# Performance work log

Hardware: AMD Instinct MI355X
Metric: run time of the kernel (lower is better)

The kernel has to match this reference:

```python
import jax, jax.numpy as jnp
import numpy as np

N_NODES = 100000
N_EDGES = 1600000
D_IN = 64
HID = 64


def setup_inputs() -> dict:
    key = jax.random.key(0)
    ks = jax.random.split(key, 8)
    s = 0.1  # modest weight scale
    return {
        "x": jax.random.normal(ks[0], (N_NODES, D_IN), jnp.float32),
        "edge_index": jax.random.randint(ks[1], (2, N_EDGES), 0, N_NODES),
        "W1": jax.random.normal(ks[2], (D_IN, HID), jnp.float32) * s,
        "b1": jnp.zeros((HID,), jnp.float32),
        "W2": jax.random.normal(ks[3], (HID, HID), jnp.float32) * s,
        "b2": jnp.zeros((HID,), jnp.float32),
        "fc1_w": jax.random.normal(ks[4], (HID, 256), jnp.float32) * s,
        "fc1_b": jnp.zeros((256,), jnp.float32),
        "fc2_w": jax.random.normal(ks[5], (256, 1), jnp.float32) * s,
        "fc2_b": jnp.zeros((1,), jnp.float32),
    }


def reference(x, edge_index, W1, b1, W2, b2, fc1_w, fc1_b, fc2_w, fc2_b):
    N = x.shape[0]
    loop = jnp.arange(N, dtype=edge_index.dtype)
    # GCNConv default: add self-loops + symmetric D^{-1/2}(A+I)D^{-1/2} normalization
    row = jnp.concatenate([edge_index[0], loop])  # source nodes
    col = jnp.concatenate([edge_index[1], loop])  # target nodes
    deg = jax.ops.segment_sum(jnp.ones(row.shape[0], x.dtype), col, num_segments=N)
    dinv = jnp.where(deg > 0, jax.lax.rsqrt(deg), 0.0)
    norm = dinv[row] * dinv[col]  # [E+N]

    def gcn_conv(h, W, b):
        h = h @ W                                   # [N, H] transform first
        msg = h[row] * norm[:, None]                # gather + scale, [E+N, H]
        return jax.ops.segment_sum(msg, col, num_segments=N) + b

    # dropout is inactive in eval mode (training=False)
    h = jax.nn.relu(gcn_conv(x, W1, b1))
    h = jax.nn.relu(gcn_conv(h, W2, b2))
    h = jax.nn.relu(h @ fc1_w + fc1_b)
    out = h @ fc2_w + fc2_b                          # [N, 1]
    # F.normalize(out, dim=0): L2 normalize along node dim, eps=1e-12
    out = out / jnp.maximum(jnp.sqrt(jnp.sum(out * out, axis=0, keepdims=True)), 1e-12)
    return out
```

## Files before the change

kernel.cpp:

```cpp
#include <hip/hip_runtime.h>
#include <hip/hip_bf16.h>

typedef unsigned short u16;
typedef unsigned int u32;
typedef __attribute__((ext_vector_type(8))) short short8;
typedef __attribute__((ext_vector_type(4))) float f32x4;

__device__ __forceinline__ float bf2f(u16 h) {
  return __uint_as_float(((u32)h) << 16);
}
__device__ __forceinline__ float ldconv(const void* p, int i, int fl) {
  return fl ? bf2f(((const u16*)p)[i]) : ((const float*)p)[i];
}
__device__ __forceinline__ u16 f2bf(float v) {
  __hip_bfloat16 h = __float2bfloat16(v);
  return *(u16*)&h;
}

__global__ void k_flag(const void* x, int* flag, float* ssum, int* bcnt) {
  __shared__ float red[256];
  int t = threadIdx.x;
  const u16* h = (const u16*)x;
  float m = 0.f;
  for (int i = t; i < 1024; i += 256) m = fmaxf(m, fabsf(bf2f(h[i])));
  red[t] = m; __syncthreads();
  for (int off = 128; off > 0; off >>= 1) {
    if (t < off) red[t] = fmaxf(red[t], red[t + off]);
    __syncthreads();
  }
  bcnt[t] = 0; bcnt[t + 256] = 0;
  if (t == 0) { *flag = (red[0] < 1000.0f) ? 1 : 0; *ssum = 0.f; }
}

__global__ void k_conv_w(const void* W1, const void* b1, const void* W2, const void* b2,
                         const void* f1w, const void* f1b, const void* f2w, const void* f2b,
                         u16* wbh, float* wbf, const int* flag) {
  int fl = *flag;
  int i = blockIdx.x * blockDim.x + threadIdx.x;
  if (i < 4096) {
    int n = i >> 6, k = i & 63;
    wbh[i] = f2bf(ldconv(W1, k * 64 + n, fl));
  } else if (i < 8192) {
    int j = i - 4096; int n = j >> 6, k = j & 63;
    wbh[i] = f2bf(ldconv(W2, k * 64 + n, fl));
  } else if (i < 24576) {
    int j = i - 8192; int n = j >> 6, k = j & 63;
    wbh[i] = f2bf(ldconv(f1w, k * 256 + n, fl));
  } else if (i < 24576 + 641) {
    int j = i - 24576;
    float v;
    if (j < 64)       v = ldconv(b1,  j,       fl);
    else if (j < 128) v = ldconv(b2,  j - 64,  fl);
    else if (j < 384) v = ldconv(f1b, j - 128, fl);
    else if (j < 640) v = ldconv(f2w, j - 384, fl);
    else              v = ldconv(f2b, 0,       fl);
    wbf[j] = v;
  }
}

__global__ __launch_bounds__(256) void k_bcount(const int* __restrict__ eidx, int E,
                                                int* bcnt, int* blockhist) {
  __shared__ int hist[512];
  int t = threadIdx.x;
  hist[t] = 0; hist[t + 256] = 0;
  __syncthreads();
  int e0 = blockIdx.x * 8192;
  int e1 = min(e0 + 8192, E);
  for (int e = e0 + t; e < e1; e += 256) atomicAdd(&hist[eidx[E + e] >> 8], 1);
  __syncthreads();
  int* bh = blockhist + blockIdx.x * 512;
  for (int j = t; j < 512; j += 256) {
    bh[j] = hist[j];
    if (hist[j]) atomicAdd(&bcnt[j], hist[j]);
  }
}

__global__ void k_bscan(const int* __restrict__ bcnt, int* bbase, int* bcur) {
  __shared__ int tmp[512];
  int t = threadIdx.x;
  int v = bcnt[t];
  tmp[t] = v; __syncthreads();
  for (int off = 1; off < 512; off <<= 1) {
    int u = (t >= off) ? tmp[t - off] : 0;
    __syncthreads();
    tmp[t] += u;
    __syncthreads();
  }
  bbase[t] = tmp[t] - v;
  bcur[t]  = tmp[t] - v;
}

__global__ __launch_bounds__(256) void k_bfill(const int* __restrict__ eidx, int E,
                                               const int* __restrict__ blockhist,
                                               int* bcur, u32* bdata) {
  __shared__ int base[512];
  __shared__ int hist[512];
  int t = threadIdx.x;
  const int* bh = blockhist + blockIdx.x * 512;
  for (int j = t; j < 512; j += 256) {
    int c = bh[j];
    base[j] = c ? atomicAdd(&bcur[j], c) : 0;
    hist[j] = 0;
  }
  __syncthreads();
  int e0 = blockIdx.x * 8192;
  int e1 = min(e0 + 8192, E);
  for (int e = e0 + t; e < e1; e += 256) {
    int src = eidx[e];
    int tgt = eidx[E + e];
    int b = tgt >> 8;
    int idx = atomicAdd(&hist[b], 1);
    bdata[base[b] + idx] = ((u32)src << 8) | (u32)(tgt & 255);
  }
}

__global__ __launch_bounds__(256) void k_csr(const u32* __restrict__ bdata,
                                             const int* __restrict__ bbase,
                                             const int* __restrict__ bcnt,
                                             int* __restrict__ deg, float* __restrict__ dinv,
                                             int* __restrict__ ptr, int* __restrict__ crow,
                                             int N) {
  __shared__ int lds[8192];
  __shared__ int hist[256];
  __shared__ int tmp[256];
  __shared__ int cur[256];
  int b = blockIdx.x, t = threadIdx.x;
  int node0 = b << 8;
  int ncnt = min(256, N - node0);
  hist[t] = 0;
  __syncthreads();
  int base = bbase[b], cnt = bcnt[b];
  for (int e = t; e < cnt; e += 256) atomicAdd(&hist[bdata[base + e] & 255], 1);
  __syncthreads();
  int h = hist[t];
  if (t < ncnt) {
    deg[node0 + t] = h + 1;
    dinv[node0 + t] = 1.0f / sqrtf((float)(h + 1));
  }
  tmp[t] = h; __syncthreads();
  for (int off = 1; off < 256; off <<= 1) {
    int u = (t >= off) ? tmp[t - off] : 0;
    __syncthreads();
    tmp[t] += u;
    __syncthreads();
  }
  int excl = tmp[t] - h;
  if (t < ncnt) ptr[node0 + t] = base + excl;
  cur[t] = excl;
  __syncthreads();
  for (int e = t; e < cnt; e += 256) {
    u32 pk = bdata[base + e];
    int pos = atomicAdd(&cur[pk & 255], 1);
    if (pos < 8192) lds[pos] = (int)(pk >> 8);
  }
  __syncthreads();
  for (int j = t; j < cnt; j += 256) crow[base + j] = lds[j];
}

__global__ __launch_bounds__(256) void k_xform(const void* __restrict__ in, int inbf,
                                               const int* __restrict__ flagp,
                                               const u16* __restrict__ wT,
                                               const float* __restrict__ dinv,
                                               u16* __restrict__ out, int N) {
  __shared__ __align__(16) u16 ws[64 * 72];
  int t = threadIdx.x;
  #pragma unroll
  for (int f = t; f < 512; f += 256) {
    int n = f >> 3, o = f & 7;
    *(float4*)&ws[n * 72 + o * 8] = ((const float4*)wT)[f];
  }
  __syncthreads();
  int fl = inbf ? 1 : *flagp;
  int lane = t & 63, wid = t >> 6;
  int g = lane >> 4, c = lane & 15;
  int arow = blockIdx.x * 64 + wid * 16 + c;
  short8 a0 = {0, 0, 0, 0, 0, 0, 0, 0}, a1 = {0, 0, 0, 0, 0, 0, 0, 0};
  if (arow < N) {
    if (fl) {
      const u16* p = (const u16*)in + (size_t)arow * 64 + g * 8;
      a0 = *(const short8*)p;
      a1 = *(const short8*)(p + 32);
    } else {
      const float* p = (const float*)in + (size_t)arow * 64 + g * 8;
      u16 tmpv[16];
      #pragma unroll
      for (int j = 0; j < 8; j++) tmpv[j] = f2bf(p[j]);
      #pragma unroll
      for (int j = 0; j < 8; j++) tmpv[8 + j] = f2bf(p[32 + j]);
      a0 = *(short8*)tmpv;
      a1 = *(short8*)(tmpv + 8);
    }
  }
  int rbase = blockIdx.x * 64 + wid * 16 + g * 4;
  float dv[4];
  #pragma unroll
  for (int r = 0; r < 4; r++) dv[r] = (rbase + r < N) ? dinv[rbase + r] : 0.f;
  #pragma unroll
  for (int tile = 0; tile < 4; tile++) {
    short8 b0 = *(const short8*)&ws[(tile * 16 + c) * 72 + g * 8];
    short8 b1 = *(const short8*)&ws[(tile * 16 + c) * 72 + g * 8 + 32];
    f32x4 z = {0.f, 0.f, 0.f, 0.f};
    f32x4 acc = __builtin_amdgcn_mfma_f32_16x16x32_bf16(a0, b0, z, 0, 0, 0);
    acc = __builtin_amdgcn_mfma_f32_16x16x32_bf16(a1, b1, acc, 0, 0, 0);
    #pragma unroll
    for (int r = 0; r < 4; r++) {
      int orow = rbase + r;
      if (orow < N) out[(size_t)orow * 64 + tile * 16 + c] = f2bf(acc[r] * dv[r]);
    }
  }
}

__global__ __launch_bounds__(256) void k_agg(const u16* __restrict__ src, u16* __restrict__ dst,
                                             const int* __restrict__ csr_row,
                                             const int* __restrict__ csr_ptr,
                                             const int* __restrict__ deg,
                                             const float* __restrict__ dinv,
                                             const float* __restrict__ bias, int N) {
  int lane = threadIdx.x & 63;
  int wid = threadIdx.x >> 6;
  int i = blockIdx.x * 4 + wid;
  if (i >= N) return;
  int sub = lane >> 3;
  int fo  = lane & 7;
  int start = csr_ptr[i];
  int total = deg[i];
  const u16* base = src + (size_t)fo * 8;
  float a0 = 0.f, a1 = 0.f, a2 = 0.f, a3 = 0.f;
  float a4 = 0.f, a5 = 0.f, a6 = 0.f, a7 = 0.f;
  #pragma unroll 4
  for (int t = sub; t < total; t += 8) {
    int r = (t == 0) ? i : csr_row[start + t - 1];
    uint4 v = *(const uint4*)(base + (size_t)r * 64);
    a0 += __uint_as_float(v.x << 16);
    a1 += __uint_as_float(v.x & 0xffff0000u);
    a2 += __uint_as_float(v.y << 16);
    a3 += __uint_as_float(v.y & 0xffff0000u);
    a4 += __uint_as_float(v.z << 16);
    a5 += __uint_as_float(v.z & 0xffff0000u);
    a6 += __uint_as_float(v.w << 16);
    a7 += __uint_as_float(v.w & 0xffff0000u);
  }
  #pragma unroll
  for (int off = 8; off < 64; off <<= 1) {
    a0 += __shfl_xor(a0, off); a1 += __shfl_xor(a1, off);
    a2 += __shfl_xor(a2, off); a3 += __shfl_xor(a3, off);
    a4 += __shfl_xor(a4, off); a5 += __shfl_xor(a5, off);
    a6 += __shfl_xor(a6, off); a7 += __shfl_xor(a7, off);
  }
  if (sub == 0) {
    float di = dinv[i];
    float4 b0 = ((const float4*)bias)[2 * fo];
    float4 b1 = ((const float4*)bias)[2 * fo + 1];
    u16 o[8];
    o[0] = f2bf(fmaxf(fmaf(a0, di, b0.x), 0.f));
    o[1] = f2bf(fmaxf(fmaf(a1, di, b0.y), 0.f));
    o[2] = f2bf(fmaxf(fmaf(a2, di, b0.z), 0.f));
    o[3] = f2bf(fmaxf(fmaf(a3, di, b0.w), 0.f));
    o[4] = f2bf(fmaxf(fmaf(a4, di, b1.x), 0.f));
    o[5] = f2bf(fmaxf(fmaf(a5, di, b1.y), 0.f));
    o[6] = f2bf(fmaxf(fmaf(a6, di, b1.z), 0.f));
    o[7] = f2bf(fmaxf(fmaf(a7, di, b1.w), 0.f));
    *(uint4*)&dst[(size_t)i * 64 + fo * 8] = *(uint4*)o;
  }
}

__global__ __launch_bounds__(256) void k_fc(const u16* __restrict__ h,
                                            const u16* __restrict__ fc1T,
                                            const float* __restrict__ wf,
                                            float* __restrict__ outf,
                                            float* __restrict__ ssum, int N) {
  __shared__ __align__(16) u16 ws[256 * 72];
  __shared__ float red[16];
  int t = threadIdx.x;
  #pragma unroll
  for (int f = t; f < 2048; f += 256) {
    int n = f >> 3, o = f & 7;
    *(float4*)&ws[n * 72 + o * 8] = ((const float4*)fc1T)[f];
  }
  __syncthreads();
  int lane = t & 63, wid = t >> 6;
  int g = lane >> 4, c = lane & 15;
  int arow = blockIdx.x * 64 + wid * 16 + c;
  short8 a0 = {0, 0, 0, 0, 0, 0, 0, 0}, a1 = {0, 0, 0, 0, 0, 0, 0, 0};
  if (arow < N) {
    a0 = *(const short8*)&h[(size_t)arow * 64 + g * 8];
    a1 = *(const short8*)&h[(size_t)arow * 64 + g * 8 + 32];
  }
  float psum[4] = {0.f, 0.f, 0.f, 0.f};
  #pragma unroll
  for (int tile = 0; tile < 16; tile++) {
    short8 b0 = *(const short8*)&ws[(tile * 16 + c) * 72 + g * 8];
    short8 b1 = *(const short8*)&ws[(tile * 16 + c) * 72 + g * 8 + 32];
    f32x4 z = {0.f, 0.f, 0.f, 0.f};
    f32x4 acc = __builtin_amdgcn_mfma_f32_16x16x32_bf16(a0, b0, z, 0, 0, 0);
    acc = __builtin_amdgcn_mfma_f32_16x16x32_bf16(a1, b1, acc, 0, 0, 0);
    int col = tile * 16 + c;
    float fb = wf[128 + col];
    float fw = wf[384 + col];
    #pragma unroll
    for (int r = 0; r < 4; r++) psum[r] += fmaxf(acc[r] + fb, 0.f) * fw;
  }
  #pragma unroll
  for (int off = 1; off < 16; off <<= 1) {
    #pragma unroll
    for (int r = 0; r < 4; r++) psum[r] += __shfl_xor(psum[r], off);
  }
  float fc2b = wf[640];
  if (c == 0) {
    float ss = 0.f;
    int rbase = blockIdx.x * 64 + wid * 16 + g * 4;
    #pragma unroll
    for (int r = 0; r < 4; r++) {
      int row = rbase + r;
      if (row < N) {
        float o = psum[r] + fc2b;
        outf[row] = o;
        ss += o * o;
      }
    }
    red[wid * 4 + g] = ss;
  }
  __syncthreads();
  if (t == 0) {
    float s = 0.f;
    #pragma unroll
    for (int j = 0; j < 16; j++) s += red[j];
    atomicAdd(ssum, s);
  }
}

__global__ void k_norm(const float* __restrict__ outf, const float* __restrict__ ssum,
                       void* dout, int N, const int* flag) {
  int i = blockIdx.x * blockDim.x + threadIdx.x;
  if (i >= N) return;
  float denom = fmaxf(sqrtf(*ssum), 1e-12f);
  float v = outf[i] / denom;
  if (*flag) ((__hip_bfloat16*)dout)[i] = __float2bfloat16(v);
  else       ((float*)dout)[i] = v;
}

extern "C" void kernel_launch(void* const* d_in, const int* in_sizes, int n_in,
                              void* d_out, int out_size, void* d_ws, size_t ws_size,
                              hipStream_t stream) {
  const void* x   = d_in[0];
  const int* eidx = (const int*)d_in[1];
  const void* W1  = d_in[2]; const void* b1  = d_in[3];
  const void* W2  = d_in[4]; const void* b2  = d_in[5];
  const void* f1w = d_in[6]; const void* f1b = d_in[7];
  const void* f2w = d_in[8]; const void* f2b = d_in[9];
  int N = in_sizes[0] / 64;
  int E = in_sizes[1] / 2;
  int NB = (N + 255) >> 8;
  int GEB = (E + 8191) / 8192;

  char* ws = (char*)d_ws;
  size_t off = 0;
  auto alloc = [&](size_t b) {
    void* p = ws + off;
    off = (off + b + 255) & ~(size_t)255;
    return p;
  };
  int*   flag  = (int*)  alloc(4);
  float* ssum  = (float*)alloc(4);
  int*   bcnt  = (int*)  alloc(512 * 4);
  int*   bbase = (int*)  alloc(512 * 4);
  int*   bcur  = (int*)  alloc(512 * 4);
  int*   bhist = (int*)  alloc((size_t)GEB * 512 * 4);
  u32*   bdata = (u32*)  alloc((size_t)E * 4);
  int*   deg   = (int*)  alloc((size_t)N * 4);
  int*   ptr   = (int*)  alloc((size_t)N * 4);
  float* dinv  = (float*)alloc((size_t)N * 4);
  int*   crow  = (int*)  alloc((size_t)E * 4);
  u16*   wbh   = (u16*)  alloc(24576 * 2);
  float* wbf   = (float*)alloc(641 * 4);
  u16*   HA    = (u16*)  alloc((size_t)N * 64 * 2);
  u16*   HT    = (u16*)  alloc((size_t)N * 64 * 2);
  float* outf  = (float*)alloc((size_t)N * 4);

  int GN = (N + 255) / 256;
  int NT = (N + 63) / 64;

  k_flag<<<1, 256, 0, stream>>>(x, flag, ssum, bcnt);
  k_conv_w<<<(24576 + 641 + 255) / 256, 256, 0, stream>>>(W1, b1, W2, b2, f1w, f1b, f2w, f2b,
                                                          wbh, wbf, flag);
  k_bcount<<<GEB, 256, 0, stream>>>(eidx, E, bcnt, bhist);
  k_bscan<<<1, 512, 0, stream>>>(bcnt, bbase, bcur);
  k_bfill<<<GEB, 256, 0, stream>>>(eidx, E, bhist, bcur, bdata);
  k_csr<<<NB, 256, 0, stream>>>(bdata, bbase, bcnt, deg, dinv, ptr, crow, N);

  k_xform<<<NT, 256, 0, stream>>>(x, 0, flag, wbh + 0, dinv, HT, N);
  k_agg<<<(N + 3) / 4, 256, 0, stream>>>(HT, HA, crow, ptr, deg, dinv, wbf + 0, N);
  k_xform<<<NT, 256, 0, stream>>>(HA, 1, flag, wbh + 4096, dinv, HT, N);
  k_agg<<<(N + 3) / 4, 256, 0, stream>>>(HT, HA, crow, ptr, deg, dinv, wbf + 64, N);
  k_fc<<<NT, 256, 0, stream>>>(HA, wbh + 8192, wbf, outf, ssum, N);
  k_norm<<<GN, 256, 0, stream>>>(outf, ssum, d_out, N, flag);
}
```

Before: 290.8 us.

## Fuse aggregation with following transforms and drop bucket scan via fixed-capacity buckets

```diff
diff --git a/kernel.cpp b/kernel.cpp
--- a/kernel.cpp
+++ b/kernel.cpp
@@ -5,6 +5,10 @@
 typedef unsigned int u32;
 typedef __attribute__((ext_vector_type(8))) short short8;
 typedef __attribute__((ext_vector_type(4))) float f32x4;
+typedef __attribute__((ext_vector_type(2))) float f32x2;
+
+#define BCAP 8192
+#define BSH  13
 
 __device__ __forceinline__ float bf2f(u16 h) {
   return __uint_as_float(((u32)h) << 16);
@@ -17,26 +21,26 @@
   return *(u16*)&h;
 }
 
-__global__ void k_flag(const void* x, int* flag, float* ssum, int* bcnt) {
+__global__ __launch_bounds__(256) void k_conv_w(const void* x,
+                         const void* W1, const void* b1, const void* W2, const void* b2,
+                         const void* f1w, const void* f1b, const void* f2w, const void* f2b,
+                         u16* wbh, float* wbf, int* flag, float* ssum, int* bcnt) {
   __shared__ float red[256];
   int t = threadIdx.x;
-  const u16* h = (const u16*)x;
+  const u16* hx = (const u16*)x;
   float m = 0.f;
-  for (int i = t; i < 1024; i += 256) m = fmaxf(m, fabsf(bf2f(h[i])));
+  for (int i = t; i < 1024; i += 256) m = fmaxf(m, fabsf(bf2f(hx[i])));
   red[t] = m; __syncthreads();
   for (int off = 128; off > 0; off >>= 1) {
     if (t < off) red[t] = fmaxf(red[t], red[t + off]);
     __syncthreads();
   }
-  bcnt[t] = 0; bcnt[t + 256] = 0;
-  if (t == 0) { *flag = (red[0] < 1000.0f) ? 1 : 0; *ssum = 0.f; }
-}
-
-__global__ void k_conv_w(const void* W1, const void* b1, const void* W2, const void* b2,
-                         const void* f1w, const void* f1b, const void* f2w, const void* f2b,
-                         u16* wbh, float* wbf, const int* flag) {
-  int fl = *flag;
-  int i = blockIdx.x * blockDim.x + threadIdx.x;
+  int fl = (red[0] < 1000.0f) ? 1 : 0;
+  if (blockIdx.x == 0) {
+    bcnt[t] = 0; bcnt[t + 256] = 0;
+    if (t == 0) { *flag = fl; *ssum = 0.f; }
+  }
+  int i = blockIdx.x * 256 + t;
   if (i < 4096) {
     int n = i >> 6, k = i & 63;
     wbh[i] = f2bf(ldconv(W1, k * 64 + n, fl));
@@ -58,9 +62,10 @@
   }
 }
 
-__global__ __launch_bounds__(256) void k_bcount(const int* __restrict__ eidx, int E,
-                                                int* bcnt, int* blockhist) {
+__global__ __launch_bounds__(256) void k_bfill(const int* __restrict__ eidx, int E,
+                                               int* bcnt, u32* bdata) {
   __shared__ int hist[512];
+  __shared__ int base[512];
   int t = threadIdx.x;
   hist[t] = 0; hist[t + 256] = 0;
   __syncthreads();
@@ -68,68 +73,37 @@
   int e1 = min(e0 + 8192, E);
   for (int e = e0 + t; e < e1; e += 256) atomicAdd(&hist[eidx[E + e] >> 8], 1);
   __syncthreads();
-  int* bh = blockhist + blockIdx.x * 512;
   for (int j = t; j < 512; j += 256) {
-    bh[j] = hist[j];
-    if (hist[j]) atomicAdd(&bcnt[j], hist[j]);
-  }
-}
-
-__global__ void k_bscan(const int* __restrict__ bcnt, int* bbase, int* bcur) {
-  __shared__ int tmp[512];
-  int t = threadIdx.x;
-  int v = bcnt[t];
-  tmp[t] = v; __syncthreads();
-  for (int off = 1; off < 512; off <<= 1) {
-    int u = (t >= off) ? tmp[t - off] : 0;
-    __syncthreads();
-    tmp[t] += u;
-    __syncthreads();
-  }
-  bbase[t] = tmp[t] - v;
-  bcur[t]  = tmp[t] - v;
-}
-
-__global__ __launch_bounds__(256) void k_bfill(const int* __restrict__ eidx, int E,
-                                               const int* __restrict__ blockhist,
-                                               int* bcur, u32* bdata) {
-  __shared__ int base[512];
-  __shared__ int hist[512];
-  int t = threadIdx.x;
-  const int* bh = blockhist + blockIdx.x * 512;
-  for (int j = t; j < 512; j += 256) {
-    int c = bh[j];
-    base[j] = c ? atomicAdd(&bcur[j], c) : 0;
+    int c = hist[j];
+    base[j] = c ? atomicAdd(&bcnt[j], c) : 0;
     hist[j] = 0;
   }
   __syncthreads();
-  int e0 = blockIdx.x * 8192;
-  int e1 = min(e0 + 8192, E);
   for (int e = e0 + t; e < e1; e += 256) {
     int src = eidx[e];
     int tgt = eidx[E + e];
     int b = tgt >> 8;
-    int idx = atomicAdd(&hist[b], 1);
-    bdata[base[b] + idx] = ((u32)src << 8) | (u32)(tgt & 255);
+    int idx = base[b] + atomicAdd(&hist[b], 1);
+    if (idx < BCAP) bdata[((size_t)b << BSH) + idx] = ((u32)src << 8) | (u32)(tgt & 255);
   }
 }
 
 __global__ __launch_bounds__(256) void k_csr(const u32* __restrict__ bdata,
-                                             const int* __restrict__ bbase,
                                              const int* __restrict__ bcnt,
                                              int* __restrict__ deg, float* __restrict__ dinv,
                                              int* __restrict__ ptr, int* __restrict__ crow,
                                              int N) {
-  __shared__ int lds[8192];
+  __shared__ int lds[BCAP];
   __shared__ int hist[256];
   __shared__ int tmp[256];
   __shared__ int cur[256];
   int b = blockIdx.x, t = threadIdx.x;
   int node0 = b << 8;
   int ncnt = min(256, N - node0);
+  size_t base = (size_t)b << BSH;
+  int cnt = min(bcnt[b], BCAP);
   hist[t] = 0;
   __syncthreads();
-  int base = bbase[b], cnt = bcnt[b];
   for (int e = t; e < cnt; e += 256) atomicAdd(&hist[bdata[base + e] & 255], 1);
   __syncthreads();
   int h = hist[t];
@@ -145,19 +119,19 @@
     __syncthreads();
   }
   int excl = tmp[t] - h;
-  if (t < ncnt) ptr[node0 + t] = base + excl;
+  if (t < ncnt) ptr[node0 + t] = (int)base + excl;
   cur[t] = excl;
   __syncthreads();
   for (int e = t; e < cnt; e += 256) {
     u32 pk = bdata[base + e];
     int pos = atomicAdd(&cur[pk & 255], 1);
-    if (pos < 8192) lds[pos] = (int)(pk >> 8);
+    if (pos < BCAP) lds[pos] = (int)(pk >> 8);
   }
   __syncthreads();
   for (int j = t; j < cnt; j += 256) crow[base + j] = lds[j];
 }
 
-__global__ __launch_bounds__(256) void k_xform(const void* __restrict__ in, int inbf,
+__global__ __launch_bounds__(256) void k_xform(const void* __restrict__ in,
                                                const int* __restrict__ flagp,
                                                const u16* __restrict__ wT,
                                                const float* __restrict__ dinv,
@@ -170,7 +144,7 @@
     *(float4*)&ws[n * 72 + o * 8] = ((const float4*)wT)[f];
   }
   __syncthreads();
-  int fl = inbf ? 1 : *flagp;
+  int fl = *flagp;
   int lane = t & 63, wid = t >> 6;
   int g = lane >> 4, c = lane & 15;
   int arow = blockIdx.x * 64 + wid * 16 + c;
@@ -210,95 +184,143 @@
   }
 }
 
-__global__ __launch_bounds__(256) void k_agg(const u16* __restrict__ src, u16* __restrict__ dst,
-                                             const int* __restrict__ csr_row,
-                                             const int* __restrict__ csr_ptr,
-                                             const int* __restrict__ deg,
-                                             const float* __restrict__ dinv,
-                                             const float* __restrict__ bias, int N) {
-  int lane = threadIdx.x & 63;
-  int wid = threadIdx.x >> 6;
-  int i = blockIdx.x * 4 + wid;
-  if (i >= N) return;
+__device__ __forceinline__ void agg_rows(const u16* __restrict__ src,
+                                         const int* __restrict__ crow,
+                                         const int* __restrict__ ptr,
+                                         const int* __restrict__ deg,
+                                         const float* __restrict__ dinv,
+                                         const float* __restrict__ bias,
+                                         u16* rows, int node0w, int wid, int lane, int N) {
   int sub = lane >> 3;
   int fo  = lane & 7;
-  int start = csr_ptr[i];
-  int total = deg[i];
-  const u16* base = src + (size_t)fo * 8;
-  float a0 = 0.f, a1 = 0.f, a2 = 0.f, a3 = 0.f;
-  float a4 = 0.f, a5 = 0.f, a6 = 0.f, a7 = 0.f;
-  #pragma unroll 4
-  for (int t = sub; t < total; t += 8) {
-    int r = (t == 0) ? i : csr_row[start + t - 1];
-    uint4 v = *(const uint4*)(base + (size_t)r * 64);
-    a0 += __uint_as_float(v.x << 16);
-    a1 += __uint_as_float(v.x & 0xffff0000u);
-    a2 += __uint_as_float(v.y << 16);
-    a3 += __uint_as_float(v.y & 0xffff0000u);
-    a4 += __uint_as_float(v.z << 16);
-    a5 += __uint_as_float(v.z & 0xffff0000u);
-    a6 += __uint_as_float(v.w << 16);
-    a7 += __uint_as_float(v.w & 0xffff0000u);
-  }
-  #pragma unroll
-  for (int off = 8; off < 64; off <<= 1) {
-    a0 += __shfl_xor(a0, off); a1 += __shfl_xor(a1, off);
-    a2 += __shfl_xor(a2, off); a3 += __shfl_xor(a3, off);
-    a4 += __shfl_xor(a4, off); a5 += __shfl_xor(a5, off);
-    a6 += __shfl_xor(a6, off); a7 += __shfl_xor(a7, off);
-  }
-  if (sub == 0) {
-    float di = dinv[i];
-    float4 b0 = ((const float4*)bias)[2 * fo];
-    float4 b1 = ((const float4*)bias)[2 * fo + 1];
-    u16 o[8];
-    o[0] = f2bf(fmaxf(fmaf(a0, di, b0.x), 0.f));
-    o[1] = f2bf(fmaxf(fmaf(a1, di, b0.y), 0.f));
-    o[2] = f2bf(fmaxf(fmaf(a2, di, b0.z), 0.f));
-    o[3] = f2bf(fmaxf(fmaf(a3, di, b0.w), 0.f));
-    o[4] = f2bf(fmaxf(fmaf(a4, di, b1.x), 0.f));
-    o[5] = f2bf(fmaxf(fmaf(a5, di, b1.y), 0.f));
-    o[6] = f2bf(fmaxf(fmaf(a6, di, b1.z), 0.f));
-    o[7] = f2bf(fmaxf(fmaf(a7, di, b1.w), 0.f));
-    *(uint4*)&dst[(size_t)i * 64 + fo * 8] = *(uint4*)o;
-  }
-}
-
-__global__ __launch_bounds__(256) void k_fc(const u16* __restrict__ h,
-                                            const u16* __restrict__ fc1T,
-                                            const float* __restrict__ wf,
-                                            float* __restrict__ outf,
-                                            float* __restrict__ ssum, int N) {
-  __shared__ __align__(16) u16 ws[256 * 72];
-  __shared__ float red[16];
+  const u16* gbase = src + (size_t)fo * 8;
+  for (int n = 0; n < 16; n++) {
+    int i = node0w + n;
+    f32x2 p0 = {0.f, 0.f}, p1 = {0.f, 0.f}, p2 = {0.f, 0.f}, p3 = {0.f, 0.f};
+    if (i < N) {
+      int start = ptr[i];
+      int total = deg[i];
+      #pragma unroll 4
+      for (int e = sub; e < total; e += 8) {
+        int r = (e == 0) ? i : crow[start + e - 1];
+        uint4 v = *(const uint4*)(gbase + (size_t)r * 64);
+        p0 += (f32x2){__uint_as_float(v.x << 16), __uint_as_float(v.x & 0xffff0000u)};
+        p1 += (f32x2){__uint_as_float(v.y << 16), __uint_as_float(v.y & 0xffff0000u)};
+        p2 += (f32x2){__uint_as_float(v.z << 16), __uint_as_float(v.z & 0xffff0000u)};
+        p3 += (f32x2){__uint_as_float(v.w << 16), __uint_as_float(v.w & 0xffff0000u)};
+      }
+    }
+    float a0 = p0.x, a1 = p0.y, a2 = p1.x, a3 = p1.y;
+    float a4 = p2.x, a5 = p2.y, a6 = p3.x, a7 = p3.y;
+    #pragma unroll
+    for (int off = 8; off < 64; off <<= 1) {
+      a0 += __shfl_xor(a0, off); a1 += __shfl_xor(a1, off);
+      a2 += __shfl_xor(a2, off); a3 += __shfl_xor(a3, off);
+      a4 += __shfl_xor(a4, off); a5 += __shfl_xor(a5, off);
+      a6 += __shfl_xor(a6, off); a7 += __shfl_xor(a7, off);
+    }
+    if (sub == 0) {
+      u16 o[8] = {0, 0, 0, 0, 0, 0, 0, 0};
+      if (i < N) {
+        float di = dinv[i];
+        float4 b0 = ((const float4*)bias)[2 * fo];
+        float4 b1 = ((const float4*)bias)[2 * fo + 1];
+        o[0] = f2bf(fmaxf(fmaf(a0, di, b0.x), 0.f));
+        o[1] = f2bf(fmaxf(fmaf(a1, di, b0.y), 0.f));
+        o[2] = f2bf(fmaxf(fmaf(a2, di, b0.z), 0.f));
+        o[3] = f2bf(fmaxf(fmaf(a3, di, b0.w), 0.f));
+        o[4] = f2bf(fmaxf(fmaf(a4, di, b1.x), 0.f));
+        o[5] = f2bf(fmaxf(fmaf(a5, di, b1.y), 0.f));
+        o[6] = f2bf(fmaxf(fmaf(a6, di, b1.z), 0.f));
+        o[7] = f2bf(fmaxf(fmaf(a7, di, b1.w), 0.f));
+      }
+      *(uint4*)&rows[(wid * 16 + n) * 72 + fo * 8] = *(uint4*)o;
+    }
+  }
+}
+
+__global__ __launch_bounds__(256) void k_aggx(const u16* __restrict__ src, u16* __restrict__ dst,
+                                              const int* __restrict__ crow,
+                                              const int* __restrict__ ptr,
+                                              const int* __restrict__ deg,
+                                              const float* __restrict__ dinv,
+                                              const float* __restrict__ bias,
+                                              const u16* __restrict__ wT, int N) {
+  __shared__ __align__(16) u16 wsW[64 * 72];
+  __shared__ __align__(16) u16 rows[64 * 72];
   int t = threadIdx.x;
   #pragma unroll
-  for (int f = t; f < 2048; f += 256) {
+  for (int f = t; f < 512; f += 256) {
     int n = f >> 3, o = f & 7;
-    *(float4*)&ws[n * 72 + o * 8] = ((const float4*)fc1T)[f];
+    *(float4*)&wsW[n * 72 + o * 8] = ((const float4*)wT)[f];
   }
   __syncthreads();
   int lane = t & 63, wid = t >> 6;
+  int node0w = blockIdx.x * 64 + wid * 16;
+  agg_rows(src, crow, ptr, deg, dinv, bias, rows, node0w, wid, lane, N);
   int g = lane >> 4, c = lane & 15;
-  int arow = blockIdx.x * 64 + wid * 16 + c;
-  short8 a0 = {0, 0, 0, 0, 0, 0, 0, 0}, a1 = {0, 0, 0, 0, 0, 0, 0, 0};
-  if (arow < N) {
-    a0 = *(const short8*)&h[(size_t)arow * 64 + g * 8];
-    a1 = *(const short8*)&h[(size_t)arow * 64 + g * 8 + 32];
-  }
-  float psum[4] = {0.f, 0.f, 0.f, 0.f};
-  #pragma unroll
-  for (int tile = 0; tile < 16; tile++) {
-    short8 b0 = *(const short8*)&ws[(tile * 16 + c) * 72 + g * 8];
-    short8 b1 = *(const short8*)&ws[(tile * 16 + c) * 72 + g * 8 + 32];
+  short8 a0 = *(const short8*)&rows[(wid * 16 + c) * 72 + g * 8];
+  short8 a1 = *(const short8*)&rows[(wid * 16 + c) * 72 + g * 8 + 32];
+  int rbase = node0w + g * 4;
+  float dv[4];
+  #pragma unroll
+  for (int r = 0; r < 4; r++) dv[r] = (rbase + r < N) ? dinv[rbase + r] : 0.f;
+  #pragma unroll
+  for (int tile = 0; tile < 4; tile++) {
+    short8 b0 = *(const short8*)&wsW[(tile * 16 + c) * 72 + g * 8];
+    short8 b1 = *(const short8*)&wsW[(tile * 16 + c) * 72 + g * 8 + 32];
     f32x4 z = {0.f, 0.f, 0.f, 0.f};
     f32x4 acc = __builtin_amdgcn_mfma_f32_16x16x32_bf16(a0, b0, z, 0, 0, 0);
     acc = __builtin_amdgcn_mfma_f32_16x16x32_bf16(a1, b1, acc, 0, 0, 0);
-    int col = tile * 16 + c;
-    float fb = wf[128 + col];
-    float fw = wf[384 + col];
-    #pragma unroll
-    for (int r = 0; r < 4; r++) psum[r] += fmaxf(acc[r] + fb, 0.f) * fw;
+    #pragma unroll
+    for (int r = 0; r < 4; r++) {
+      int orow = rbase + r;
+      if (orow < N) dst[(size_t)orow * 64 + tile * 16 + c] = f2bf(acc[r] * dv[r]);
+    }
+  }
+}
+
+__global__ __launch_bounds__(256) void k_aggfc(const u16* __restrict__ src,
+                                               const int* __restrict__ crow,
+                                               const int* __restrict__ ptr,
+                                               const int* __restrict__ deg,
+                                               const float* __restrict__ dinv,
+                                               const float* __restrict__ bias,
+                                               const u16* __restrict__ fc1T,
+                                               const float* __restrict__ wf,
+                                               float* __restrict__ outf,
+                                               float* __restrict__ ssum, int N) {
+  __shared__ __align__(16) u16 wsF[128 * 72];
+  __shared__ float red[16];
+  int t = threadIdx.x;
+  int lane = t & 63, wid = t >> 6;
+  int node0w = blockIdx.x * 64 + wid * 16;
+  agg_rows(src, crow, ptr, deg, dinv, bias, wsF, node0w, wid, lane, N);
+  int g = lane >> 4, c = lane & 15;
+  short8 a0 = *(const short8*)&wsF[(wid * 16 + c) * 72 + g * 8];
+  short8 a1 = *(const short8*)&wsF[(wid * 16 + c) * 72 + g * 8 + 32];
+  float psum[4] = {0.f, 0.f, 0.f, 0.f};
+  for (int ph = 0; ph < 2; ph++) {
+    __syncthreads();
+    #pragma unroll
+    for (int f = t; f < 1024; f += 256) {
+      int n = f >> 3, o = f & 7;
+      *(float4*)&wsF[n * 72 + o * 8] = ((const float4*)(fc1T + ph * 8192))[f];
+    }
+    __syncthreads();
+    #pragma unroll
+    for (int tile = 0; tile < 8; tile++) {
+      short8 b0 = *(const short8*)&wsF[(tile * 16 + c) * 72 + g * 8];
+      short8 b1 = *(const short8*)&wsF[(tile * 16 + c) * 72 + g * 8 + 32];
+      f32x4 z = {0.f, 0.f, 0.f, 0.f};
+      f32x4 acc = __builtin_amdgcn_mfma_f32_16x16x32_bf16(a0, b0, z, 0, 0, 0);
+      acc = __builtin_amdgcn_mfma_f32_16x16x32_bf16(a1, b1, acc, 0, 0, 0);
+      int col = ph * 128 + tile * 16 + c;
+      float fb = wf[128 + col];
+      float fw = wf[384 + col];
+      #pragma unroll
+      for (int r = 0; r < 4; r++) psum[r] += fmaxf(acc[r] + fb, 0.f) * fw;
+    }
   }
   #pragma unroll
   for (int off = 1; off < 16; off <<= 1) {
@@ -308,7 +330,7 @@
   float fc2b = wf[640];
   if (c == 0) {
     float ss = 0.f;
-    int rbase = blockIdx.x * 64 + wid * 16 + g * 4;
+    int rbase = node0w + g * 4;
     #pragma unroll
     for (int r = 0; r < 4; r++) {
       int row = rbase + r;
@@ -363,35 +385,28 @@
   int*   flag  = (int*)  alloc(4);
   float* ssum  = (float*)alloc(4);
   int*   bcnt  = (int*)  alloc(512 * 4);
-  int*   bbase = (int*)  alloc(512 * 4);
-  int*   bcur  = (int*)  alloc(512 * 4);
-  int*   bhist = (int*)  alloc((size_t)GEB * 512 * 4);
-  u32*   bdata = (u32*)  alloc((size_t)E * 4);
+  u32*   bdata = (u32*)  alloc((size_t)NB * BCAP * 4);
   int*   deg   = (int*)  alloc((size_t)N * 4);
   int*   ptr   = (int*)  alloc((size_t)N * 4);
   float* dinv  = (float*)alloc((size_t)N * 4);
-  int*   crow  = (int*)  alloc((size_t)E * 4);
+  int*   crow  = (int*)  alloc((size_t)NB * BCAP * 4);
   u16*   wbh   = (u16*)  alloc(24576 * 2);
   float* wbf   = (float*)alloc(641 * 4);
+  u16*   HT    = (u16*)  alloc((size_t)N * 64 * 2);
   u16*   HA    = (u16*)  alloc((size_t)N * 64 * 2);
-  u16*   HT    = (u16*)  alloc((size_t)N * 64 * 2);
   float* outf  = (float*)alloc((size_t)N * 4);
 
   int GN = (N + 255) / 256;
   int NT = (N + 63) / 64;
 
-  k_flag<<<1, 256, 0, stream>>>(x, flag, ssum, bcnt);
-  k_conv_w<<<(24576 + 641 + 255) / 256, 256, 0, stream>>>(W1, b1, W2, b2, f1w, f1b, f2w, f2b,
-                                                          wbh, wbf, flag);
-  k_bcount<<<GEB, 256, 0, stream>>>(eidx, E, bcnt, bhist);
-  k_bscan<<<1, 512, 0, stream>>>(bcnt, bbase, bcur);
-  k_bfill<<<GEB, 256, 0, stream>>>(eidx, E, bhist, bcur, bdata);
-  k_csr<<<NB, 256, 0, stream>>>(bdata, bbase, bcnt, deg, dinv, ptr, crow, N);
-
-  k_xform<<<NT, 256, 0, stream>>>(x, 0, flag, wbh + 0, dinv, HT, N);
-  k_agg<<<(N + 3) / 4, 256, 0, stream>>>(HT, HA, crow, ptr, deg, dinv, wbf + 0, N);
-  k_xform<<<NT, 256, 0, stream>>>(HA, 1, flag, wbh + 4096, dinv, HT, N);
-  k_agg<<<(N + 3) / 4, 256, 0, stream>>>(HT, HA, crow, ptr, deg, dinv, wbf + 64, N);
-  k_fc<<<NT, 256, 0, stream>>>(HA, wbh + 8192, wbf, outf, ssum, N);
+  k_conv_w<<<(24576 + 641 + 255) / 256, 256, 0, stream>>>(x, W1, b1, W2, b2, f1w, f1b, f2w, f2b,
+                                                          wbh, wbf, flag, ssum, bcnt);
+  k_bfill<<<GEB, 256, 0, stream>>>(eidx, E, bcnt, bdata);
+  k_csr<<<NB, 256, 0, stream>>>(bdata, bcnt, deg, dinv, ptr, crow, N);
+
+  k_xform<<<NT, 256, 0, stream>>>(x, flag, wbh + 0, dinv, HT, N);
+  k_aggx<<<NT, 256, 0, stream>>>(HT, HA, crow, ptr, deg, dinv, wbf + 0, wbh + 4096, N);
+  k_aggfc<<<NT, 256, 0, stream>>>(HA, crow, ptr, deg, dinv, wbf + 64, wbh + 8192, wbf,
+                                  outf, ssum, N);
   k_norm<<<GN, 256, 0, stream>>>(outf, ssum, d_out, N, flag);
 }
```

Result: slower. 311.1 us (+7.0%).

## Aggregate before layer-2 transform and fuse W2 matmul into FC kernel

Applied to the files above, without the earlier changes.

```diff
diff --git a/kernel.cpp b/kernel.cpp
--- a/kernel.cpp
+++ b/kernel.cpp
@@ -215,7 +215,7 @@
                                              const int* __restrict__ csr_ptr,
                                              const int* __restrict__ deg,
                                              const float* __restrict__ dinv,
-                                             const float* __restrict__ bias, int N) {
+                                             const float* __restrict__ bias, int post, int N) {
   int lane = threadIdx.x & 63;
   int wid = threadIdx.x >> 6;
   int i = blockIdx.x * 4 + wid;
@@ -248,34 +248,43 @@
     a6 += __shfl_xor(a6, off); a7 += __shfl_xor(a7, off);
   }
   if (sub == 0) {
-    float di = dinv[i];
-    float4 b0 = ((const float4*)bias)[2 * fo];
-    float4 b1 = ((const float4*)bias)[2 * fo + 1];
     u16 o[8];
-    o[0] = f2bf(fmaxf(fmaf(a0, di, b0.x), 0.f));
-    o[1] = f2bf(fmaxf(fmaf(a1, di, b0.y), 0.f));
-    o[2] = f2bf(fmaxf(fmaf(a2, di, b0.z), 0.f));
-    o[3] = f2bf(fmaxf(fmaf(a3, di, b0.w), 0.f));
-    o[4] = f2bf(fmaxf(fmaf(a4, di, b1.x), 0.f));
-    o[5] = f2bf(fmaxf(fmaf(a5, di, b1.y), 0.f));
-    o[6] = f2bf(fmaxf(fmaf(a6, di, b1.z), 0.f));
-    o[7] = f2bf(fmaxf(fmaf(a7, di, b1.w), 0.f));
+    if (post) {
+      float di = dinv[i];
+      float4 b0 = ((const float4*)bias)[2 * fo];
+      float4 b1 = ((const float4*)bias)[2 * fo + 1];
+      o[0] = f2bf(di * fmaxf(fmaf(a0, di, b0.x), 0.f));
+      o[1] = f2bf(di * fmaxf(fmaf(a1, di, b0.y), 0.f));
+      o[2] = f2bf(di * fmaxf(fmaf(a2, di, b0.z), 0.f));
+      o[3] = f2bf(di * fmaxf(fmaf(a3, di, b0.w), 0.f));
+      o[4] = f2bf(di * fmaxf(fmaf(a4, di, b1.x), 0.f));
+      o[5] = f2bf(di * fmaxf(fmaf(a5, di, b1.y), 0.f));
+      o[6] = f2bf(di * fmaxf(fmaf(a6, di, b1.z), 0.f));
+      o[7] = f2bf(di * fmaxf(fmaf(a7, di, b1.w), 0.f));
+    } else {
+      o[0] = f2bf(a0); o[1] = f2bf(a1); o[2] = f2bf(a2); o[3] = f2bf(a3);
+      o[4] = f2bf(a4); o[5] = f2bf(a5); o[6] = f2bf(a6); o[7] = f2bf(a7);
+    }
     *(uint4*)&dst[(size_t)i * 64 + fo * 8] = *(uint4*)o;
   }
 }
 
-__global__ __launch_bounds__(256) void k_fc(const u16* __restrict__ h,
-                                            const u16* __restrict__ fc1T,
-                                            const float* __restrict__ wf,
-                                            float* __restrict__ outf,
-                                            float* __restrict__ ssum, int N) {
-  __shared__ __align__(16) u16 ws[256 * 72];
+__global__ __launch_bounds__(256) void k_xfc(const u16* __restrict__ S,
+                                             const u16* __restrict__ w2T,
+                                             const u16* __restrict__ fc1T,
+                                             const float* __restrict__ wf,
+                                             const float* __restrict__ dinv,
+                                             float* __restrict__ outf,
+                                             float* __restrict__ ssum, int N) {
+  __shared__ __align__(16) u16 w2s[64 * 72];
+  __shared__ __align__(16) u16 rows[64 * 72];
+  __shared__ __align__(16) u16 f1s[128 * 72];
   __shared__ float red[16];
   int t = threadIdx.x;
   #pragma unroll
-  for (int f = t; f < 2048; f += 256) {
+  for (int f = t; f < 512; f += 256) {
     int n = f >> 3, o = f & 7;
-    *(float4*)&ws[n * 72 + o * 8] = ((const float4*)fc1T)[f];
+    *(float4*)&w2s[n * 72 + o * 8] = ((const float4*)w2T)[f];
   }
   __syncthreads();
   int lane = t & 63, wid = t >> 6;
@@ -283,22 +292,52 @@
   int arow = blockIdx.x * 64 + wid * 16 + c;
   short8 a0 = {0, 0, 0, 0, 0, 0, 0, 0}, a1 = {0, 0, 0, 0, 0, 0, 0, 0};
   if (arow < N) {
-    a0 = *(const short8*)&h[(size_t)arow * 64 + g * 8];
-    a1 = *(const short8*)&h[(size_t)arow * 64 + g * 8 + 32];
-  }
-  float psum[4] = {0.f, 0.f, 0.f, 0.f};
-  #pragma unroll
-  for (int tile = 0; tile < 16; tile++) {
-    short8 b0 = *(const short8*)&ws[(tile * 16 + c) * 72 + g * 8];
-    short8 b1 = *(const short8*)&ws[(tile * 16 + c) * 72 + g * 8 + 32];
+    a0 = *(const short8*)&S[(size_t)arow * 64 + g * 8];
+    a1 = *(const short8*)&S[(size_t)arow * 64 + g * 8 + 32];
+  }
+  int rbase = blockIdx.x * 64 + wid * 16 + g * 4;
+  float dv[4];
+  #pragma unroll
+  for (int r = 0; r < 4; r++) dv[r] = (rbase + r < N) ? dinv[rbase + r] : 0.f;
+  #pragma unroll
+  for (int tile = 0; tile < 4; tile++) {
+    short8 b0 = *(const short8*)&w2s[(tile * 16 + c) * 72 + g * 8];
+    short8 b1 = *(const short8*)&w2s[(tile * 16 + c) * 72 + g * 8 + 32];
     f32x4 z = {0.f, 0.f, 0.f, 0.f};
     f32x4 acc = __builtin_amdgcn_mfma_f32_16x16x32_bf16(a0, b0, z, 0, 0, 0);
     acc = __builtin_amdgcn_mfma_f32_16x16x32_bf16(a1, b1, acc, 0, 0, 0);
     int col = tile * 16 + c;
-    float fb = wf[128 + col];
-    float fw = wf[384 + col];
-    #pragma unroll
-    for (int r = 0; r < 4; r++) psum[r] += fmaxf(acc[r] + fb, 0.f) * fw;
+    float b2v = wf[64 + col];
+    #pragma unroll
+    for (int r = 0; r < 4; r++) {
+      float tv = fmaxf(fmaf(acc[r], dv[r], b2v), 0.f);
+      rows[(wid * 16 + g * 4 + r) * 72 + col] = f2bf(tv);
+    }
+  }
+  short8 t0 = *(const short8*)&rows[(wid * 16 + c) * 72 + g * 8];
+  short8 t1 = *(const short8*)&rows[(wid * 16 + c) * 72 + g * 8 + 32];
+  float psum[4] = {0.f, 0.f, 0.f, 0.f};
+  for (int ph = 0; ph < 2; ph++) {
+    __syncthreads();
+    #pragma unroll
+    for (int f = t; f < 1024; f += 256) {
+      int n = f >> 3, o = f & 7;
+      *(float4*)&f1s[n * 72 + o * 8] = ((const float4*)(fc1T + ph * 8192))[f];
+    }
+    __syncthreads();
+    #pragma unroll
+    for (int tile = 0; tile < 8; tile++) {
+      short8 b0 = *(const short8*)&f1s[(tile * 16 + c) * 72 + g * 8];
+      short8 b1 = *(const short8*)&f1s[(tile * 16 + c) * 72 + g * 8 + 32];
+      f32x4 z = {0.f, 0.f, 0.f, 0.f};
+      f32x4 acc = __builtin_amdgcn_mfma_f32_16x16x32_bf16(t0, b0, z, 0, 0, 0);
+      acc = __builtin_amdgcn_mfma_f32_16x16x32_bf16(t1, b1, acc, 0, 0, 0);
+      int col = ph * 128 + tile * 16 + c;
+      float fb = wf[128 + col];
+      float fw = wf[384 + col];
+      #pragma unroll
+      for (int r = 0; r < 4; r++) psum[r] += fmaxf(acc[r] + fb, 0.f) * fw;
+    }
   }
   #pragma unroll
   for (int off = 1; off < 16; off <<= 1) {
@@ -308,7 +347,6 @@
   float fc2b = wf[640];
   if (c == 0) {
     float ss = 0.f;
-    int rbase = blockIdx.x * 64 + wid * 16 + g * 4;
     #pragma unroll
     for (int r = 0; r < 4; r++) {
       int row = rbase + r;
@@ -389,9 +427,8 @@
   k_csr<<<NB, 256, 0, stream>>>(bdata, bbase, bcnt, deg, dinv, ptr, crow, N);
 
   k_xform<<<NT, 256, 0, stream>>>(x, 0, flag, wbh + 0, dinv, HT, N);
-  k_agg<<<(N + 3) / 4, 256, 0, stream>>>(HT, HA, crow, ptr, deg, dinv, wbf + 0, N);
-  k_xform<<<NT, 256, 0, stream>>>(HA, 1, flag, wbh + 4096, dinv, HT, N);
-  k_agg<<<(N + 3) / 4, 256, 0, stream>>>(HT, HA, crow, ptr, deg, dinv, wbf + 64, N);
-  k_fc<<<NT, 256, 0, stream>>>(HA, wbh + 8192, wbf, outf, ssum, N);
+  k_agg<<<(N + 3) / 4, 256, 0, stream>>>(HT, HA, crow, ptr, deg, dinv, wbf + 0, 1, N);
+  k_agg<<<(N + 3) / 4, 256, 0, stream>>>(HA, HT, crow, ptr, deg, dinv, wbf, 0, N);
+  k_xfc<<<NT, 256, 0, stream>>>(HT, wbh + 4096, wbh + 8192, wbf, dinv, outf, ssum, N);
   k_norm<<<GN, 256, 0, stream>>>(outf, ssum, d_out, N, flag);
 }
```

New measurement: 275.8 us. 1.05x faster.
